# Performance work log

Hardware: AMD Instinct MI355X
Metric: run time of the kernel (lower is better)

## Reference

```python
import jax, jax.numpy as jnp
import numpy as np

N = 100000      # nodes
E = 1600000     # edges (before self-loops)
IN_DIM = 128
HID = 32
HEADS = 4
EMB = 128
SLOPE = 0.2     # PyG GATConv default negative_slope


def setup_inputs() -> dict:
    key = jax.random.key(0)
    ks = jax.random.split(key, 16)
    def glorot(k, shape):
        fan_in = shape[0] if len(shape) > 1 else shape[-1]
        return jax.random.normal(k, shape, jnp.float32) * (1.0 / np.sqrt(fan_in))
    x = jax.random.normal(ks[0], (N, IN_DIM), jnp.float32)
    edge_index = jax.random.randint(ks[1], (2, E), 0, N)
    return {
        "x": x,
        "edge_index": edge_index,
        # layer 1: in_dim -> hidden (heads=4, concat)
        "W1": glorot(ks[2], (IN_DIM, HEADS * HID)),
        "att_src1": glorot(ks[3], (HEADS, HID)),
        "att_dst1": glorot(ks[4], (HEADS, HID)),
        "b1": jnp.zeros((HEADS * HID,), jnp.float32),
        # layer 2: hidden*heads -> hidden (heads=4, concat)
        "W2": glorot(ks[5], (HEADS * HID, HEADS * HID)),
        "att_src2": glorot(ks[6], (HEADS, HID)),
        "att_dst2": glorot(ks[7], (HEADS, HID)),
        "b2": jnp.zeros((HEADS * HID,), jnp.float32),
        # layer 3: hidden*heads -> embed (heads=1)
        "W3": glorot(ks[8], (HEADS * HID, EMB)),
        "att_src3": glorot(ks[9], (1, EMB)),
        "att_dst3": glorot(ks[10], (1, EMB)),
        "b3": jnp.zeros((EMB,), jnp.float32),
    }


def gat_conv(x, src, dst, W, att_src, att_dst, b, heads, out_ch):
    """One PyG-style GATConv (concat=True). src/dst already include self-loops."""
    n = x.shape[0]
    h = (x @ W).reshape(n, heads, out_ch)                 # [N,H,C]
    a_s = jnp.einsum('nhc,hc->nh', h, att_src)            # [N,H]
    a_d = jnp.einsum('nhc,hc->nh', h, att_dst)            # [N,H]
    e = jax.nn.leaky_relu(a_s[src] + a_d[dst], SLOPE)     # [E',H]
    # numerically stable softmax over irregular incoming neighborhoods (per dst)
    m = jax.ops.segment_max(e, dst, num_segments=n)       # [N,H]
    ex = jnp.exp(e - m[dst])
    denom = jax.ops.segment_sum(ex, dst, num_segments=n)  # [N,H]
    alpha = ex / denom[dst]                                # [E',H]
    out = jax.ops.segment_sum(h[src] * alpha[:, :, None], dst, num_segments=n)
    return out.reshape(n, heads * out_ch) + b


def reference(x, edge_index, W1, att_src1, att_dst1, b1,
              W2, att_src2, att_dst2, b2, W3, att_src3, att_dst3, b3):
    n = x.shape[0]
    loops = jnp.arange(n, dtype=edge_index.dtype)
    src = jnp.concatenate([edge_index[0], loops])  # PyG add_self_loops=True
    dst = jnp.concatenate([edge_index[1], loops])
    h = gat_conv(x, src, dst, W1, att_src1, att_dst1, b1, HEADS, HID)
    h = jax.nn.elu(h)
    h = gat_conv(h, src, dst, W2, att_src2, att_dst2, b2, HEADS, HID)
    h = jax.nn.elu(h)
    out = gat_conv(h, src, dst, W3, att_src3, att_dst3, b3, 1, EMB)
    return out
```

## Files before the change

### kernel.cpp

```cpp
#include <hip/hip_runtime.h>
#include <hip/hip_fp16.h>
#include <math.h>

#define N_NODES 100000
#define N_EDGES 1600000
#define SLOPE 0.2f

#define BSHIFT 8
#define NB 391
#define CHUNK 8192

typedef _Float16 f16x8 __attribute__((ext_vector_type(8)));
typedef float f32x4 __attribute__((ext_vector_type(4)));

__global__ __launch_bounds__(256) void partA1(const int* __restrict__ ei,
                                              int* __restrict__ bucket_count,
                                              int E, int n) {
  __shared__ int cnt[NB];
  for (int i = threadIdx.x; i < NB; i += 256) cnt[i] = 0;
  __syncthreads();
  int base = blockIdx.x * CHUNK;
  int total = E + n;
  int lim = min(base + CHUNK, total);
  for (int e = base + threadIdx.x; e < lim; e += 256) {
    int d = (e < E) ? ei[E + e] : (e - E);
    atomicAdd(&cnt[d >> BSHIFT], 1);
  }
  __syncthreads();
  for (int i = threadIdx.x; i < NB; i += 256)
    if (cnt[i]) atomicAdd(&bucket_count[i], cnt[i]);
}

__global__ __launch_bounds__(512) void scan_nb(
    const int* __restrict__ bucket_count, int* __restrict__ bucket_base,
    int* __restrict__ bucket_cursor) {
  __shared__ int lds[512];
  int t = threadIdx.x;
  int v = (t < NB) ? bucket_count[t] : 0;
  int x = v;
  lds[t] = x;
  __syncthreads();
  for (int off = 1; off < 512; off <<= 1) {
    int y = (t >= off) ? lds[t - off] : 0;
    __syncthreads();
    x += y;
    lds[t] = x;
    __syncthreads();
  }
  int excl = x - v;
  if (t <= NB) bucket_base[t] = excl;
  if (t < NB) bucket_cursor[t] = excl;
}

__global__ __launch_bounds__(256) void partA2(const int* __restrict__ ei,
                                              int* __restrict__ bucket_cursor,
                                              unsigned* __restrict__ part,
                                              int E, int n) {
  __shared__ int cnt[NB];
  __shared__ int res[NB];
  for (int i = threadIdx.x; i < NB; i += 256) cnt[i] = 0;
  __syncthreads();
  int base = blockIdx.x * CHUNK;
  int total = E + n;
  int lim = min(base + CHUNK, total);
  for (int e = base + threadIdx.x; e < lim; e += 256) {
    int d = (e < E) ? ei[E + e] : (e - E);
    atomicAdd(&cnt[d >> BSHIFT], 1);
  }
  __syncthreads();
  for (int i = threadIdx.x; i < NB; i += 256)
    res[i] = cnt[i] ? atomicAdd(&bucket_cursor[i], cnt[i]) : 0;
  __syncthreads();
  for (int e = base + threadIdx.x; e < lim; e += 256) {
    int s, d;
    if (e < E) { s = ei[e]; d = ei[E + e]; } else { s = d = e - E; }
    int b = d >> BSHIFT;
    int pos = atomicAdd(&res[b], 1);
    part[pos] = ((unsigned)s << BSHIFT) | (unsigned)(d & 255);
  }
}

__global__ __launch_bounds__(256) void passB(const unsigned* __restrict__ part,
                                             const int* __restrict__ bucket_base,
                                             int* __restrict__ row_start,
                                             int* __restrict__ edge_src, int n) {
  __shared__ int cnt[256];
  __shared__ int sc[256];
  __shared__ int loff[256];
  int b = blockIdx.x;
  int t = threadIdx.x;
  int node0 = b << BSHIFT;
  int bstart = bucket_base[b], bend = bucket_base[b + 1];
  cnt[t] = 0;
  __syncthreads();
  for (int i = bstart + t; i < bend; i += 256)
    atomicAdd(&cnt[part[i] & 255], 1);
  __syncthreads();
  int v = cnt[t];
  int x = v;
  sc[t] = x;
  __syncthreads();
  for (int off = 1; off < 256; off <<= 1) {
    int y = (t >= off) ? sc[t - off] : 0;
    __syncthreads();
    x += y;
    sc[t] = x;
    __syncthreads();
  }
  int excl = x - v;
  loff[t] = excl;
  int node = node0 + t;
  if (node < n) row_start[node] = bstart + excl;
  if (b == NB - 1 && t == 0) row_start[n] = bucket_base[NB];
  __syncthreads();
  for (int i = bstart + t; i < bend; i += 256) {
    unsigned p = part[i];
    int dl = p & 255;
    int pos = bstart + atomicAdd(&loff[dl], 1);
    edge_src[pos] = (int)(p >> BSHIFT);
  }
}

__global__ __launch_bounds__(256) void convert_w(
    const float* __restrict__ W1, const float* __restrict__ W2,
    const float* __restrict__ W3, __half* __restrict__ Wt1,
    __half* __restrict__ Wt2, __half* __restrict__ Wt3) {
  int idx = blockIdx.x * 256 + threadIdx.x;
  if (idx >= 3 * 16384) return;
  int mat = idx >> 14;
  int r = idx & 16383;
  int k = r >> 7, col = r & 127;
  const float* W = (mat == 0) ? W1 : (mat == 1) ? W2 : W3;
  __half* Wt = (mat == 0) ? Wt1 : (mat == 1) ? Wt2 : Wt3;
  Wt[col * 128 + k] = __float2half(W[k * 128 + col]);
}

template <int H, typename InT>
__global__ __launch_bounds__(256) void gemm_att_mfma(
    const InT* __restrict__ X, const __half* __restrict__ Wt,
    const float* __restrict__ att_src, const float* __restrict__ att_dst,
    __half* __restrict__ Y, float* __restrict__ a_s, float* __restrict__ a_d,
    int n) {
  __shared__ _Float16 A_lds[64 * 128];
  __shared__ _Float16 B_lds[128 * 128];
  int t = threadIdx.x;
  int r0 = blockIdx.x * 64;

  {
    int row = t >> 2;
    int c0 = (t & 3) * 32;
    bool inb = (r0 + row) < n;
    if constexpr (sizeof(InT) == 4) {
      const float* xp = (const float*)X + (size_t)(r0 + row) * 128 + c0;
#pragma unroll
      for (int i = 0; i < 8; i++) {
        float4 v;
        if (inb) v = *(const float4*)(xp + i * 4);
        else v = make_float4(0.f, 0.f, 0.f, 0.f);
        union { float2 f; __half2 h2[2]; } u;
        u.h2[0] = __floats2half2_rn(v.x, v.y);
        u.h2[1] = __floats2half2_rn(v.z, v.w);
        *(float2*)&A_lds[row * 128 + c0 + i * 4] = u.f;
      }
    } else {
      const __half* xp = (const __half*)X + (size_t)(r0 + row) * 128 + c0;
#pragma unroll
      for (int i = 0; i < 4; i++) {
        float4 v;
        if (inb) v = *(const float4*)(xp + i * 8);
        else v = make_float4(0.f, 0.f, 0.f, 0.f);
        *(float4*)&A_lds[row * 128 + c0 + i * 8] = v;
      }
    }
  }
  {
    const __half* wp = Wt + t * 64;
#pragma unroll
    for (int i = 0; i < 8; i++)
      *(float4*)&B_lds[t * 64 + i * 8] = *(const float4*)(wp + i * 8);
  }
  __syncthreads();

  int wv = t >> 6, lane = t & 63, quad = lane >> 4, l15 = lane & 15;
  const _Float16* Arow = &A_lds[(wv * 16 + l15) * 128];
  f32x4 acc[8];
#pragma unroll
  for (int ct = 0; ct < 8; ct++) acc[ct] = (f32x4){0.f, 0.f, 0.f, 0.f};

#pragma unroll
  for (int kb = 0; kb < 4; kb++) {
    f16x8 a = *(const f16x8*)(Arow + kb * 32 + quad * 8);
#pragma unroll
    for (int ct = 0; ct < 8; ct++) {
      f16x8 b = *(const f16x8*)(&B_lds[(ct * 16 + l15) * 128 + kb * 32 + quad * 8]);
      acc[ct] = __builtin_amdgcn_mfma_f32_16x16x32_f16(a, b, acc[ct], 0, 0, 0);
    }
  }

  int rbase = r0 + wv * 16 + quad * 4;
#pragma unroll
  for (int reg = 0; reg < 4; reg++) {
    int row = rbase + reg;
    if (row < n) {
#pragma unroll
      for (int ct = 0; ct < 8; ct++)
        Y[(size_t)row * 128 + ct * 16 + l15] = __float2half(acc[ct][reg]);
    }
  }

  float avs[8], avd[8];
#pragma unroll
  for (int ct = 0; ct < 8; ct++) {
    avs[ct] = att_src[ct * 16 + l15];
    avd[ct] = att_dst[ct * 16 + l15];
  }
  if constexpr (H == 4) {
    float ps[4][4], pd_[4][4];
#pragma unroll
    for (int hd = 0; hd < 4; hd++)
#pragma unroll
      for (int reg = 0; reg < 4; reg++) { ps[hd][reg] = 0.f; pd_[hd][reg] = 0.f; }
#pragma unroll
    for (int ct = 0; ct < 8; ct++) {
      int hd = ct >> 1;
#pragma unroll
      for (int reg = 0; reg < 4; reg++) {
        ps[hd][reg] = fmaf(acc[ct][reg], avs[ct], ps[hd][reg]);
        pd_[hd][reg] = fmaf(acc[ct][reg], avd[ct], pd_[hd][reg]);
      }
    }
#pragma unroll
    for (int off = 1; off <= 8; off <<= 1)
#pragma unroll
      for (int hd = 0; hd < 4; hd++)
#pragma unroll
        for (int reg = 0; reg < 4; reg++) {
          ps[hd][reg] += __shfl_xor(ps[hd][reg], off, 64);
          pd_[hd][reg] += __shfl_xor(pd_[hd][reg], off, 64);
        }
#pragma unroll
    for (int hd = 0; hd < 4; hd++)
      if (l15 == hd) {
#pragma unroll
        for (int reg = 0; reg < 4; reg++) {
          int row = rbase + reg;
          if (row < n) {
            a_s[row * 4 + hd] = ps[hd][reg];
            a_d[row * 4 + hd] = pd_[hd][reg];
          }
        }
      }
  } else {
    float ps[4] = {}, pd_[4] = {};
#pragma unroll
    for (int ct = 0; ct < 8; ct++)
#pragma unroll
      for (int reg = 0; reg < 4; reg++) {
        ps[reg] = fmaf(acc[ct][reg], avs[ct], ps[reg]);
        pd_[reg] = fmaf(acc[ct][reg], avd[ct], pd_[reg]);
      }
#pragma unroll
    for (int off = 1; off <= 8; off <<= 1)
#pragma unroll
      for (int reg = 0; reg < 4; reg++) {
        ps[reg] += __shfl_xor(ps[reg], off, 64);
        pd_[reg] += __shfl_xor(pd_[reg], off, 64);
      }
    if (l15 == 0) {
#pragma unroll
      for (int reg = 0; reg < 4; reg++) {
        int row = rbase + reg;
        if (row < n) { a_s[row] = ps[reg]; a_d[row] = pd_[reg]; }
      }
    }
  }
}

template <int H, bool DO_ELU, typename OutT>
__global__ __launch_bounds__(256) void agg_kernel(
    const __half* __restrict__ h, const float* __restrict__ a_s,
    const float* __restrict__ a_d, const int* __restrict__ row_start,
    const int* __restrict__ edge_src, const float* __restrict__ bias,
    OutT* __restrict__ out, int n) {
  const int C = 128 / H;
  __shared__ float w_lds[4][H * 66];
  __shared__ int sn_lds[4][64];
  int wslot = threadIdx.x >> 6;
  int wid = (blockIdx.x * blockDim.x + threadIdx.x) >> 6;
  int lane = threadIdx.x & 63;
  if (wid >= n) return;
  int start = row_start[wid], end = row_start[wid + 1];
  int deg = end - start;

  float adv[H];
#pragma unroll
  for (int hh = 0; hh < H; hh++) adv[hh] = a_d[wid * H + hh];

  if (deg <= 64) {
    bool valid = lane < deg;
    int sn = valid ? edge_src[start + lane] : 0;
    float e[H];
    if (valid) {
      if constexpr (H == 4) {
        float4 asv = *(const float4*)(a_s + (size_t)sn * 4);
        float t0 = asv.x + adv[0];
        float t1 = asv.y + adv[1];
        float t2 = asv.z + adv[2];
        float t3 = asv.w + adv[3];
        e[0] = t0 >= 0.f ? t0 : SLOPE * t0;
        e[1] = t1 >= 0.f ? t1 : SLOPE * t1;
        e[2] = t2 >= 0.f ? t2 : SLOPE * t2;
        e[3] = t3 >= 0.f ? t3 : SLOPE * t3;
      } else {
        float tt = a_s[sn] + adv[0];
        e[0] = tt >= 0.f ? tt : SLOPE * tt;
      }
    } else {
#pragma unroll
      for (int hh = 0; hh < H; hh++) e[hh] = -1e30f;
    }
    bool small = (deg <= 32);
    float w[H], s[H];
#pragma unroll
    for (int hh = 0; hh < H; hh++) {
      w[hh] = valid ? __expf(e[hh] - 40.f) : 0.f;
      s[hh] = w[hh];
    }
#pragma unroll
    for (int off = 1; off <= 16; off <<= 1)
#pragma unroll
      for (int hh = 0; hh < H; hh++) s[hh] += __shfl_xor(s[hh], off, 64);
    if (!small)
#pragma unroll
      for (int hh = 0; hh < H; hh++) s[hh] += __shfl_xor(s[hh], 32, 64);
    sn_lds[wslot][lane] = sn << 8;
#pragma unroll
    for (int hh = 0; hh < H; hh++)
      w_lds[wslot][hh * 66 + lane] = valid ? w[hh] * (1.f / s[hh]) : 0.f;
    __builtin_amdgcn_wave_barrier();

    int g = lane >> 4, l = lane & 15;
    int d0 = l * 8;
    int dby = l * 16;
    int headBase = (H == 4) ? (l >> 2) * 66 : 0;
    float acc[8];
#pragma unroll
    for (int k = 0; k < 8; k++) acc[k] = 0.f;
    int degp16 = (deg + 15) & ~15;
    for (int eidx = 0; eidx < degp16; eidx += 16) {
#pragma unroll
      for (int jj = 0; jj < 4; jj++) {
        int ei2 = eidx + jj * 4 + g;
        int boff = sn_lds[wslot][ei2] + dby;
        float wv = w_lds[wslot][headBase + ei2];
        union { float4 f; __half2 h2[4]; } u;
        u.f = *(const float4*)((const char*)h + (unsigned)boff);
        float2 p0 = __half22float2(u.h2[0]);
        float2 p1 = __half22float2(u.h2[1]);
        float2 p2 = __half22float2(u.h2[2]);
        float2 p3 = __half22float2(u.h2[3]);
        acc[0] = fmaf(p0.x, wv, acc[0]);
        acc[1] = fmaf(p0.y, wv, acc[1]);
        acc[2] = fmaf(p1.x, wv, acc[2]);
        acc[3] = fmaf(p1.y, wv, acc[3]);
        acc[4] = fmaf(p2.x, wv, acc[4]);
        acc[5] = fmaf(p2.y, wv, acc[5]);
        acc[6] = fmaf(p3.x, wv, acc[6]);
        acc[7] = fmaf(p3.y, wv, acc[7]);
      }
    }
#pragma unroll
    for (int k = 0; k < 8; k++) {
      acc[k] += __shfl_xor(acc[k], 16, 64);
      acc[k] += __shfl_xor(acc[k], 32, 64);
    }
    if (lane < 16) {
      float4 bv0 = *(const float4*)(bias + d0);
      float4 bv1 = *(const float4*)(bias + d0 + 4);
      float o[8];
      o[0] = acc[0] + bv0.x; o[1] = acc[1] + bv0.y;
      o[2] = acc[2] + bv0.z; o[3] = acc[3] + bv0.w;
      o[4] = acc[4] + bv1.x; o[5] = acc[5] + bv1.y;
      o[6] = acc[6] + bv1.z; o[7] = acc[7] + bv1.w;
      if (DO_ELU) {
#pragma unroll
        for (int k = 0; k < 8; k++)
          o[k] = (o[k] > 0.f) ? o[k] : __expf(o[k]) - 1.f;
      }
      if constexpr (sizeof(OutT) == 2) {
        union { float4 f4; __half2 h2[4]; } uo;
        uo.h2[0] = __floats2half2_rn(o[0], o[1]);
        uo.h2[1] = __floats2half2_rn(o[2], o[3]);
        uo.h2[2] = __floats2half2_rn(o[4], o[5]);
        uo.h2[3] = __floats2half2_rn(o[6], o[7]);
        *(float4*)((__half*)out + (size_t)wid * 128 + d0) = uo.f4;
      } else {
        float4 ov0 = {o[0], o[1], o[2], o[3]};
        float4 ov1 = {o[4], o[5], o[6], o[7]};
        *(float4*)((float*)out + (size_t)wid * 128 + d0) = ov0;
        *(float4*)((float*)out + (size_t)wid * 128 + d0 + 4) = ov1;
      }
    }
    return;
  }

  {
    const int G = C / 2;
    int head = lane / G;
    float m[H], s[H];
#pragma unroll
    for (int hh = 0; hh < H; hh++) { m[hh] = -1e30f; s[hh] = 0.f; }
    for (int idx = start + lane; idx < end; idx += 64) {
      int sn = edge_src[idx];
#pragma unroll
      for (int hh = 0; hh < H; hh++) {
        float e = a_s[sn * H + hh] + adv[hh];
        e = (e >= 0.f) ? e : SLOPE * e;
        float mn = fmaxf(m[hh], e);
        s[hh] = s[hh] * __expf(m[hh] - mn) + __expf(e - mn);
        m[hh] = mn;
      }
    }
    for (int off = 1; off < 64; off <<= 1) {
#pragma unroll
      for (int hh = 0; hh < H; hh++) {
        float mo = __shfl_xor(m[hh], off, 64);
        float so = __shfl_xor(s[hh], off, 64);
        float mn = fmaxf(m[hh], mo);
        s[hh] = s[hh] * __expf(m[hh] - mn) + so * __expf(mo - mn);
        m[hh] = mn;
      }
    }
    int d0 = lane * 2;
    float mh = m[head];
    float rsh = 1.f / s[head];
    float adh = adv[head];
    float acc0 = 0.f, acc1 = 0.f;
    for (int idx = start; idx < end; idx++) {
      int sn = edge_src[idx];
      float e = a_s[sn * H + head] + adh;
      e = (e >= 0.f) ? e : SLOPE * e;
      float w = __expf(e - mh) * rsh;
      float2 hv = __half22float2(*(const __half2*)(h + (size_t)sn * 128 + d0));
      acc0 += w * hv.x;
      acc1 += w * hv.y;
    }
    float o0 = acc0 + bias[d0];
    float o1 = acc1 + bias[d0 + 1];
    if (DO_ELU) {
      o0 = (o0 > 0.f) ? o0 : __expf(o0) - 1.f;
      o1 = (o1 > 0.f) ? o1 : __expf(o1) - 1.f;
    }
    out[(size_t)wid * 128 + d0] = (OutT)o0;
    out[(size_t)wid * 128 + d0 + 1] = (OutT)o1;
  }
}

extern "C" void kernel_launch(void* const* d_in, const int* in_sizes, int n_in,
                              void* d_out, int out_size, void* d_ws,
                              size_t ws_size, hipStream_t stream) {
  const float* x = (const float*)d_in[0];
  const int* ei = (const int*)d_in[1];
  const float* W1 = (const float*)d_in[2];
  const float* as1 = (const float*)d_in[3];
  const float* ad1 = (const float*)d_in[4];
  const float* b1 = (const float*)d_in[5];
  const float* W2 = (const float*)d_in[6];
  const float* as2 = (const float*)d_in[7];
  const float* ad2 = (const float*)d_in[8];
  const float* b2 = (const float*)d_in[9];
  const float* W3 = (const float*)d_in[10];
  const float* as3 = (const float*)d_in[11];
  const float* ad3 = (const float*)d_in[12];
  const float* b3 = (const float*)d_in[13];
  float* out = (float*)d_out;

  const int n = N_NODES, E = N_EDGES, total = E + n;

  char* ws = (char*)d_ws;
  size_t off = 0;
  auto alloc = [&](size_t bytes) -> char* {
    char* p = ws + off;
    off = (off + bytes + 255) & ~(size_t)255;
    return p;
  };
  __half* hbuf = (__half*)alloc(sizeof(__half) * (size_t)n * 128);
  float* a_s = (float*)alloc(sizeof(float) * n * 4);
  float* a_d = (float*)alloc(sizeof(float) * n * 4);
  unsigned* part = (unsigned*)alloc(sizeof(unsigned) * total);
  int* edge_src = (int*)alloc(sizeof(int) * total);
  int* row_start = (int*)alloc(sizeof(int) * (n + 1));
  int* bucket_count = (int*)alloc(sizeof(int) * (NB + 1));
  int* bucket_base = (int*)alloc(sizeof(int) * (NB + 1));
  int* bucket_cursor = (int*)alloc(sizeof(int) * (NB + 1));
  __half* Wt1 = (__half*)alloc(sizeof(__half) * 16384);
  __half* Wt2 = (__half*)alloc(sizeof(__half) * 16384);
  __half* Wt3 = (__half*)alloc(sizeof(__half) * 16384);
  __half* hbuf2 = (__half*)alloc(sizeof(__half) * (size_t)n * 128);
  bool fp16mid = (off <= ws_size);

  hipMemsetAsync(bucket_count, 0, sizeof(int) * (NB + 1), stream);

  convert_w<<<192, 256, 0, stream>>>(W1, W2, W3, Wt1, Wt2, Wt3);

  int nblkA = (total + CHUNK - 1) / CHUNK;
  partA1<<<nblkA, 256, 0, stream>>>(ei, bucket_count, E, n);
  scan_nb<<<1, 512, 0, stream>>>(bucket_count, bucket_base, bucket_cursor);
  partA2<<<nblkA, 256, 0, stream>>>(ei, bucket_cursor, part, E, n);
  passB<<<NB, 256, 0, stream>>>(part, bucket_base, row_start, edge_src, n);

  int agg_blocks = (n + 3) / 4;
  int gemm_blocks = (n + 63) / 64;

  if (fp16mid) {
    gemm_att_mfma<4, float><<<gemm_blocks, 256, 0, stream>>>(
        x, Wt1, as1, ad1, hbuf, a_s, a_d, n);
    agg_kernel<4, true, __half><<<agg_blocks, 256, 0, stream>>>(
        hbuf, a_s, a_d, row_start, edge_src, b1, hbuf2, n);

    gemm_att_mfma<4, __half><<<gemm_blocks, 256, 0, stream>>>(
        hbuf2, Wt2, as2, ad2, hbuf, a_s, a_d, n);
    agg_kernel<4, true, __half><<<agg_blocks, 256, 0, stream>>>(
        hbuf, a_s, a_d, row_start, edge_src, b2, hbuf2, n);

    gemm_att_mfma<1, __half><<<gemm_blocks, 256, 0, stream>>>(
        hbuf2, Wt3, as3, ad3, hbuf, a_s, a_d, n);
    agg_kernel<1, false, float><<<agg_blocks, 256, 0, stream>>>(
        hbuf, a_s, a_d, row_start, edge_src, b3, out, n);
  } else {
    gemm_att_mfma<4, float><<<gemm_blocks, 256, 0, stream>>>(
        x, Wt1, as1, ad1, hbuf, a_s, a_d, n);
    agg_kernel<4, true, float><<<agg_blocks, 256, 0, stream>>>(
        hbuf, a_s, a_d, row_start, edge_src, b1, out, n);

    gemm_att_mfma<4, float><<<gemm_blocks, 256, 0, stream>>>(
        out, Wt2, as2, ad2, hbuf, a_s, a_d, n);
    agg_kernel<4, true, float><<<agg_blocks, 256, 0, stream>>>(
        hbuf, a_s, a_d, row_start, edge_src, b2, out, n);

    gemm_att_mfma<1, float><<<gemm_blocks, 256, 0, stream>>>(
        out, Wt3, as3, ad3, hbuf, a_s, a_d, n);
    agg_kernel<1, false, float><<<agg_blocks, 256, 0, stream>>>(
        hbuf, a_s, a_d, row_start, edge_src, b3, out, n);
  }
}
```

Measured before the change: 496.5 us.

## Load GEMM A operand directly to registers, swizzle B in LDS, vectorize aggregation

The GEMM kernel no longer stages the A tile through LDS. Each lane loads its MFMA A fragments straight from global memory into registers, converting to fp16 there. The B tile is stored in LDS with an XOR swizzle to avoid bank conflicts, and launch bounds ask for 4 blocks per CU. The aggregation inner loop is rewritten with vector types, with the goal of producing packed conversions and FMAs. Together these cut LDS traffic, the smaller LDS footprint raises occupancy, and register pressure goes up.

```diff
diff --git a/kernel.cpp b/kernel.cpp
--- a/kernel.cpp
+++ b/kernel.cpp
@@ -12,6 +12,7 @@
 
 typedef _Float16 f16x8 __attribute__((ext_vector_type(8)));
 typedef float f32x4 __attribute__((ext_vector_type(4)));
+typedef float f32x8v __attribute__((ext_vector_type(8)));
 
 __global__ __launch_bounds__(256) void partA1(const int* __restrict__ ei,
                                               int* __restrict__ bucket_count,
@@ -136,64 +137,67 @@
 }
 
 template <int H, typename InT>
-__global__ __launch_bounds__(256) void gemm_att_mfma(
+__global__ __launch_bounds__(256, 4) void gemm_att_mfma(
     const InT* __restrict__ X, const __half* __restrict__ Wt,
     const float* __restrict__ att_src, const float* __restrict__ att_dst,
     __half* __restrict__ Y, float* __restrict__ a_s, float* __restrict__ a_d,
     int n) {
-  __shared__ _Float16 A_lds[64 * 128];
   __shared__ _Float16 B_lds[128 * 128];
   int t = threadIdx.x;
   int r0 = blockIdx.x * 64;
-
-  {
-    int row = t >> 2;
-    int c0 = (t & 3) * 32;
-    bool inb = (r0 + row) < n;
-    if constexpr (sizeof(InT) == 4) {
-      const float* xp = (const float*)X + (size_t)(r0 + row) * 128 + c0;
-#pragma unroll
-      for (int i = 0; i < 8; i++) {
-        float4 v;
-        if (inb) v = *(const float4*)(xp + i * 4);
-        else v = make_float4(0.f, 0.f, 0.f, 0.f);
-        union { float2 f; __half2 h2[2]; } u;
-        u.h2[0] = __floats2half2_rn(v.x, v.y);
-        u.h2[1] = __floats2half2_rn(v.z, v.w);
-        *(float2*)&A_lds[row * 128 + c0 + i * 4] = u.f;
-      }
-    } else {
-      const __half* xp = (const __half*)X + (size_t)(r0 + row) * 128 + c0;
-#pragma unroll
-      for (int i = 0; i < 4; i++) {
-        float4 v;
-        if (inb) v = *(const float4*)(xp + i * 8);
-        else v = make_float4(0.f, 0.f, 0.f, 0.f);
-        *(float4*)&A_lds[row * 128 + c0 + i * 8] = v;
-      }
-    }
-  }
+  int wv = t >> 6, lane = t & 63, quad = lane >> 4, l15 = lane & 15;
+
   {
     const __half* wp = Wt + t * 64;
-#pragma unroll
-    for (int i = 0; i < 8; i++)
-      *(float4*)&B_lds[t * 64 + i * 8] = *(const float4*)(wp + i * 8);
-  }
-  __syncthreads();
-
-  int wv = t >> 6, lane = t & 63, quad = lane >> 4, l15 = lane & 15;
-  const _Float16* Arow = &A_lds[(wv * 16 + l15) * 128];
+    int brow = t >> 1;
+    int sbase = (t & 1) * 8;
+#pragma unroll
+    for (int i = 0; i < 8; i++) {
+      int slot = (sbase + i) ^ (brow & 15);
+      *(float4*)&B_lds[brow * 128 + slot * 8] = *(const float4*)(wp + i * 8);
+    }
+  }
+
+  int arow = r0 + wv * 16 + l15;
+  bool inb = arow < n;
+  f16x8 a[4];
+  if constexpr (sizeof(InT) == 4) {
+    const float* xp = (const float*)X + (size_t)arow * 128 + quad * 8;
+#pragma unroll
+    for (int kb = 0; kb < 4; kb++) {
+      float4 v0, v1;
+      if (inb) {
+        v0 = *(const float4*)(xp + kb * 32);
+        v1 = *(const float4*)(xp + kb * 32 + 4);
+      } else {
+        v0 = make_float4(0.f, 0.f, 0.f, 0.f);
+        v1 = v0;
+      }
+      f32x8v f = {v0.x, v0.y, v0.z, v0.w, v1.x, v1.y, v1.z, v1.w};
+      a[kb] = __builtin_convertvector(f, f16x8);
+    }
+  } else {
+    const __half* xp = (const __half*)X + (size_t)arow * 128 + quad * 8;
+    f16x8 z = {};
+#pragma unroll
+    for (int kb = 0; kb < 4; kb++) {
+      if (inb) a[kb] = *(const f16x8*)(xp + kb * 32);
+      else a[kb] = z;
+    }
+  }
+  __syncthreads();
+
   f32x4 acc[8];
 #pragma unroll
   for (int ct = 0; ct < 8; ct++) acc[ct] = (f32x4){0.f, 0.f, 0.f, 0.f};
 
 #pragma unroll
   for (int kb = 0; kb < 4; kb++) {
-    f16x8 a = *(const f16x8*)(Arow + kb * 32 + quad * 8);
 #pragma unroll
     for (int ct = 0; ct < 8; ct++) {
-      f16x8 b = *(const f16x8*)(&B_lds[(ct * 16 + l15) * 128 + kb * 32 + quad * 8]);
-      acc[ct] = __builtin_amdgcn_mfma_f32_16x16x32_f16(a, b, acc[ct], 0, 0, 0);
+      f16x8 b = *(const f16x8*)(
+          &B_lds[(ct * 16 + l15) * 128 + (((kb * 4 + quad) ^ l15) * 8)]);
+      acc[ct] = __builtin_amdgcn_mfma_f32_16x16x32_f16(a[kb], b, acc[ct], 0, 0, 0);
     }
   }
 
@@ -341,47 +345,35 @@
 
     int g = lane >> 4, l = lane & 15;
     int d0 = l * 8;
-    int dby = l * 16;
+    const char* hb = (const char*)h + l * 16;
     int headBase = (H == 4) ? (l >> 2) * 66 : 0;
-    float acc[8];
-#pragma unroll
-    for (int k = 0; k < 8; k++) acc[k] = 0.f;
+    f32x8v acc = {};
     int degp16 = (deg + 15) & ~15;
     for (int eidx = 0; eidx < degp16; eidx += 16) {
 #pragma unroll
       for (int jj = 0; jj < 4; jj++) {
         int ei2 = eidx + jj * 4 + g;
-        int boff = sn_lds[wslot][ei2] + dby;
+        int boff = sn_lds[wslot][ei2];
         float wv = w_lds[wslot][headBase + ei2];
-        union { float4 f; __half2 h2[4]; } u;
-        u.f = *(const float4*)((const char*)h + (unsigned)boff);
-        float2 p0 = __half22float2(u.h2[0]);
-        float2 p1 = __half22float2(u.h2[1]);
-        float2 p2 = __half22float2(u.h2[2]);
-        float2 p3 = __half22float2(u.h2[3]);
-        acc[0] = fmaf(p0.x, wv, acc[0]);
-        acc[1] = fmaf(p0.y, wv, acc[1]);
-        acc[2] = fmaf(p1.x, wv, acc[2]);
-        acc[3] = fmaf(p1.y, wv, acc[3]);
-        acc[4] = fmaf(p2.x, wv, acc[4]);
-        acc[5] = fmaf(p2.y, wv, acc[5]);
-        acc[6] = fmaf(p3.x, wv, acc[6]);
-        acc[7] = fmaf(p3.y, wv, acc[7]);
-      }
-    }
+        f16x8 hv = *(const f16x8*)(hb + (unsigned)boff);
+        f32x8v pf = __builtin_convertvector(hv, f32x8v);
+        f32x8v ws = {wv, wv, wv, wv, wv, wv, wv, wv};
+        acc = pf * ws + acc;
+      }
+    }
+    float o[8];
 #pragma unroll
     for (int k = 0; k < 8; k++) {
-      acc[k] += __shfl_xor(acc[k], 16, 64);
-      acc[k] += __shfl_xor(acc[k], 32, 64);
+      float v = acc[k];
+      v += __shfl_xor(v, 16, 64);
+      v += __shfl_xor(v, 32, 64);
+      o[k] = v;
     }
     if (lane < 16) {
       float4 bv0 = *(const float4*)(bias + d0);
       float4 bv1 = *(const float4*)(bias + d0 + 4);
-      float o[8];
-      o[0] = acc[0] + bv0.x; o[1] = acc[1] + bv0.y;
-      o[2] = acc[2] + bv0.z; o[3] = acc[3] + bv0.w;
-      o[4] = acc[4] + bv1.x; o[5] = acc[5] + bv1.y;
-      o[6] = acc[6] + bv1.z; o[7] = acc[7] + bv1.w;
+      o[0] += bv0.x; o[1] += bv0.y; o[2] += bv0.z; o[3] += bv0.w;
+      o[4] += bv1.x; o[5] += bv1.y; o[6] += bv1.z; o[7] += bv1.w;
       if (DO_ELU) {
 #pragma unroll
         for (int k = 0; k < 8; k++)
```

After: 466.4 us. -6.1%, faster.
